# Kernel optimization log

Measured on AMD Instinct MI355X. Metric: run time of the kernel, lower is better.

The kernel has to match this reference:

```python
import jax, jax.numpy as jnp
import numpy as np

NQ, NL, NPCA, NCLS = 7, 6, 32, 3129
DIM = 2 ** NQ
B = 8192

# PauliZ diagonal per wire (PennyLane convention: wire 0 = most significant bit)
_bits = (np.arange(DIM)[None, :] >> (NQ - 1 - np.arange(NQ))[:, None]) & 1
Z_DIAG = jnp.asarray(1.0 - 2.0 * _bits, dtype=jnp.float32)  # (NQ, DIM)

# CNOT(control=q, target=(q+1)%NQ) as a static basis-index permutation (involution)
def _cnot_perm(c, t):
    idx = np.arange(DIM)
    cbit = (idx >> (NQ - 1 - c)) & 1
    return jnp.asarray(idx ^ (cbit << (NQ - 1 - t)))
CNOT_PERMS = [_cnot_perm(q, (q + 1) % NQ) for q in range(NQ)]

def _apply_ry(state, q, theta):
    # state: (B, DIM) complex64; theta: (B,) per-sample or scalar
    st = state.reshape(-1, 2 ** q, 2, 2 ** (NQ - 1 - q))
    th = jnp.asarray(theta)
    c = jnp.cos(th / 2)
    s = jnp.sin(th / 2)
    if th.ndim == 1:
        c = c[:, None, None]
        s = s[:, None, None]
    a0, a1 = st[:, :, 0, :], st[:, :, 1, :]
    return jnp.stack((c * a0 - s * a1, s * a0 + c * a1), axis=2).reshape(-1, DIM)

def _apply_rz(state, q, theta):
    # RZ = diag(e^{-i t/2}, e^{+i t/2}); theta is a shared scalar here
    st = state.reshape(-1, 2 ** q, 2, 2 ** (NQ - 1 - q))
    p = jnp.exp(jnp.complex64(-0.5j) * theta)
    a0, a1 = st[:, :, 0, :], st[:, :, 1, :]
    return jnp.stack((p * a0, jnp.conj(p) * a1), axis=2).reshape(-1, DIM)

def _quantum_circuit(feats, weights):
    # feats: (B, NL*NQ) encoding angles (data re-uploading); weights: (NL, NQ, 2)
    bsz = feats.shape[0]
    state = jnp.zeros((bsz, DIM), jnp.complex64).at[:, 0].set(1.0)
    for layer in range(NL):
        for q in range(NQ):
            # RY data-encoding followed by variational RY rotate about the same axis -> fuse angles
            state = _apply_ry(state, q, feats[:, layer * NQ + q] + weights[layer, q, 0])
            state = _apply_rz(state, q, weights[layer, q, 1])
        for q in range(NQ):  # ring entanglement
            state = state[:, CNOT_PERMS[q]]
    probs = state.real ** 2 + state.imag ** 2  # (B, DIM)
    return probs @ Z_DIAG.T  # (B, NQ) <Z_i> expectation values

def setup_inputs() -> dict:
    key = jax.random.key(0)
    ks = jax.random.split(key, 8)
    def lin(k, i, o):
        return (jax.random.normal(k, (i, o), jnp.float32) / np.sqrt(i)).astype(jnp.float32)
    return {
        "x": jax.random.normal(ks[0], (B, NPCA), jnp.float32),
        "feature_scale": jnp.ones((NPCA,), jnp.float32),
        "quantum_weights": jax.random.normal(ks[1], (NL, NQ, 2), jnp.float32) * 0.1,
        "qh_w1": lin(ks[2], NQ, 64), "qh_b1": jnp.zeros((64,), jnp.float32),
        "qh_w2": lin(ks[3], 64, NCLS), "qh_b2": jnp.zeros((NCLS,), jnp.float32),
        "ch_w1": lin(ks[4], NPCA, 256), "ch_b1": jnp.zeros((256,), jnp.float32),
        "ch_w2": lin(ks[5], 256, 128), "ch_b2": jnp.zeros((128,), jnp.float32),
        "ch_w3": lin(ks[6], 128, NCLS), "ch_b3": jnp.zeros((NCLS,), jnp.float32),
    }

def reference(x, feature_scale, quantum_weights, qh_w1, qh_b1, qh_w2, qh_b2,
              ch_w1, ch_b1, ch_w2, ch_b2, ch_w3, ch_b3):
    # prepare_features: learned scale -> arctan squash -> zero-pad to NL*NQ angles
    feats = jnp.arctan(x * feature_scale)
    feats = jnp.pad(feats, ((0, 0), (0, NL * NQ - NPCA)))
    q_features = _quantum_circuit(feats, quantum_weights)          # (B, NQ)
    q_logits = jax.nn.relu(q_features @ qh_w1 + qh_b1) @ qh_w2 + qh_b2
    h = jax.nn.relu(x @ ch_w1 + ch_b1)                             # dropout = identity at eval
    h = jax.nn.relu(h @ ch_w2 + ch_b2)
    c_logits = h @ ch_w3 + ch_b3
    return (q_logits, c_logits, q_features)
```

## Files before the change

kernel.cpp:

```cpp
#include <hip/hip_runtime.h>
#include <hip/hip_bf16.h>
#include <math.h>

#define NQ 7
#define NL 6
#define BATCH 8192
#define NPCA 32
#define NCLS 3129
#define NGATE 42

#define NBQ 2048
#define NBC 512
#define NBX 49
#define NBT (3 * NBX)

#define GXB 25
#define GYB 64
#define GNB (GXB * GYB * 2)
#define GCPX (GNB / 8)

typedef __attribute__((ext_vector_type(8))) short short8;
typedef __attribute__((ext_vector_type(4))) float f32x4;

__device__ __forceinline__ void gload_lds16(const void* g, void* l) {
    __builtin_amdgcn_global_load_lds(
        (const __attribute__((address_space(1))) void*)g,
        (__attribute__((address_space(3))) void*)l, 16, 0, 0);
}

__global__ __launch_bounds__(256) void prep_kernel(
    const float* __restrict__ x,
    const float* __restrict__ fscale,
    const float* __restrict__ qw,
    const float* __restrict__ qh_w1,
    const float* __restrict__ qh_b1,
    const float* __restrict__ cw1, const float* __restrict__ cb1,
    const float* __restrict__ cw2, const float* __restrict__ cb2,
    const float* __restrict__ qw2, const float* __restrict__ cw3,
    float* __restrict__ qf_out,
    __hip_bfloat16* __restrict__ hq_out,
    __hip_bfloat16* __restrict__ h2_out,
    __hip_bfloat16* __restrict__ qw2t,
    __hip_bfloat16* __restrict__ cw3t)
{
    __shared__ alignas(16) unsigned char smem[18752];
    const int bid = blockIdx.x;
    const int tid = threadIdx.x;

    if (bid < NBQ) {
        float* pzc = (float*)smem;
        float* pzs = pzc + NGATE;
        float* w0s = pzs + NGATE;
        if (tid < NGATE) {
            float t = qw[tid * 2 + 1] * 0.5f;
            float s, c;
            sincosf(t, &s, &c);
            pzs[tid] = s; pzc[tid] = c;
            w0s[tid] = qw[tid * 2 + 0];
        }
        __syncthreads();

        const int lane = tid & 63;
        const int wave = tid >> 6;
        const int sample = bid * 4 + wave;

        float myfeat = 0.f;
        if (lane < NPCA) myfeat = atanf(x[sample * NPCA + lane] * fscale[lane]);

        float rs[NGATE - NPCA], rc[NGATE - NPCA];
        #pragma unroll
        for (int g = NPCA; g < NGATE; ++g) {
            float th = w0s[g] * 0.5f;
            rs[g - NPCA] = __sinf(th);
            rc[g - NPCA] = __cosf(th);
        }

        float s0r = (lane == 0) ? 1.f : 0.f, s0i = 0.f, s1r = 0.f, s1i = 0.f;

        #pragma unroll
        for (int layer = 0; layer < NL; ++layer) {
            #pragma unroll
            for (int q = 0; q < NQ; ++q) {
                const int g = layer * NQ + q;
                const int b = NQ - 1 - q;
                float s, c;
                if (g < NPCA) {
                    float fv = __shfl(myfeat, g);
                    float th = (fv + w0s[g]) * 0.5f;
                    s = __sinf(th); c = __cosf(th);
                } else {
                    s = rs[g - NPCA]; c = rc[g - NPCA];
                }
                if (b == 0) {
                    float n0r = c * s0r - s * s1r, n0i = c * s0i - s * s1i;
                    float n1r = s * s0r + c * s1r, n1i = s * s0i + c * s1i;
                    s0r = n0r; s0i = n0i; s1r = n1r; s1i = n1i;
                } else {
                    int m = 1 << (b - 1);
                    float p0r = __shfl_xor(s0r, m), p0i = __shfl_xor(s0i, m);
                    float p1r = __shfl_xor(s1r, m), p1i = __shfl_xor(s1i, m);
                    if (((lane >> (b - 1)) & 1) == 0) {
                        s0r = c * s0r - s * p0r; s0i = c * s0i - s * p0i;
                        s1r = c * s1r - s * p1r; s1i = c * s1i - s * p1i;
                    } else {
                        s0r = s * p0r + c * s0r; s0i = s * p0i + c * s0i;
                        s1r = s * p1r + c * s1r; s1i = s * p1i + c * s1i;
                    }
                }
                float pc = pzc[g], ps = pzs[g];
                if (b == 0) {
                    float u0 = pc * s0r + ps * s0i; s0i = pc * s0i - ps * s0r; s0r = u0;
                    float u1 = pc * s1r - ps * s1i; s1i = pc * s1i + ps * s1r; s1r = u1;
                } else {
                    float e = (((lane >> (b - 1)) & 1) == 0) ? ps : -ps;
                    float u0 = pc * s0r + e * s0i; s0i = pc * s0i - e * s0r; s0r = u0;
                    float u1 = pc * s1r + e * s1i; s1i = pc * s1i - e * s1r; s1r = u1;
                }
            }
            #pragma unroll
            for (int cq = 0; cq < NQ; ++cq) {
                if (cq == NQ - 1) {
                    float r = __shfl_xor(s1r, 32), im = __shfl_xor(s1i, 32);
                    s1r = r; s1i = im;
                } else if (cq == NQ - 2) {
                    if (lane & 1) {
                        float tr = s0r; s0r = s1r; s1r = tr;
                        float ti = s0i; s0i = s1i; s1i = ti;
                    }
                } else {
                    const int bc = NQ - 1 - cq;
                    const int bt = bc - 1;
                    int m = 1 << (bt - 1);
                    float p0r = __shfl_xor(s0r, m), p0i = __shfl_xor(s0i, m);
                    float p1r = __shfl_xor(s1r, m), p1i = __shfl_xor(s1i, m);
                    if ((lane >> (bc - 1)) & 1) {
                        s0r = p0r; s0i = p0i; s1r = p1r; s1i = p1i;
                    }
                }
            }
        }

        float p0 = s0r * s0r + s0i * s0i;
        float p1 = s1r * s1r + s1i * s1i;
        float psum = p0 + p1;
        float qf[7];
        #pragma unroll
        for (int k = 0; k < 6; ++k)
            qf[k] = (((lane >> (5 - k)) & 1) ? -psum : psum);
        qf[6] = p0 - p1;
        #pragma unroll
        for (int off = 32; off >= 1; off >>= 1) {
            #pragma unroll
            for (int k = 0; k < 7; ++k) qf[k] += __shfl_xor(qf[k], off);
        }

        float acc = qh_b1[lane];
        #pragma unroll
        for (int k = 0; k < 7; ++k) acc += qf[k] * qh_w1[k * 64 + lane];
        hq_out[sample * 64 + lane] = __float2bfloat16(fmaxf(acc, 0.f));
        if (lane < 7) qf_out[sample * 7 + lane] = qf[lane];

    } else if (bid < NBQ + NBC) {
        float (*xs)[33]   = (float(*)[33])smem;
        float (*h1s)[260] = (float(*)[260])(smem + 2112);
        const int row0 = (bid - NBQ) * 16;

        for (int i = tid; i < 16 * 32; i += 256) {
            int r = i >> 5, k = i & 31;
            xs[r][k] = x[(row0 + r) * 32 + k];
        }
        __syncthreads();

        {
            float w1c[32];
            #pragma unroll
            for (int k = 0; k < 32; ++k) w1c[k] = cw1[k * 256 + tid];
            float bb = cb1[tid];
            #pragma unroll
            for (int r = 0; r < 16; ++r) {
                float a = bb;
                #pragma unroll
                for (int k = 0; k < 32; ++k) a += xs[r][k] * w1c[k];
                h1s[r][tid] = fmaxf(a, 0.f);
            }
        }
        __syncthreads();

        {
            const int c0 = (tid & 31) * 4;
            const int r0 = (tid >> 5) * 2;
            float4 bv = *(const float4*)&cb2[c0];
            float a0[4] = {bv.x, bv.y, bv.z, bv.w};
            float a1[4] = {bv.x, bv.y, bv.z, bv.w};
            for (int k = 0; k < 256; k += 4) {
                float4 h0 = *(const float4*)&h1s[r0][k];
                float4 h1 = *(const float4*)&h1s[r0 + 1][k];
                #pragma unroll
                for (int j = 0; j < 4; ++j) {
                    float4 w = *(const float4*)&cw2[(size_t)(k + j) * 128 + c0];
                    float hv0 = (j == 0) ? h0.x : (j == 1) ? h0.y : (j == 2) ? h0.z : h0.w;
                    float hv1 = (j == 0) ? h1.x : (j == 1) ? h1.y : (j == 2) ? h1.z : h1.w;
                    a0[0] += hv0 * w.x; a0[1] += hv0 * w.y; a0[2] += hv0 * w.z; a0[3] += hv0 * w.w;
                    a1[0] += hv1 * w.x; a1[1] += hv1 * w.y; a1[2] += hv1 * w.z; a1[3] += hv1 * w.w;
                }
            }
            #pragma unroll
            for (int rr = 0; rr < 2; ++rr) {
                float* a = rr ? a1 : a0;
                __hip_bfloat162 q0, q1;
                q0.x = __float2bfloat16(fmaxf(a[0], 0.f));
                q0.y = __float2bfloat16(fmaxf(a[1], 0.f));
                q1.x = __float2bfloat16(fmaxf(a[2], 0.f));
                q1.y = __float2bfloat16(fmaxf(a[3], 0.f));
                size_t base = (size_t)(row0 + r0 + rr) * 128 + c0;
                *(__hip_bfloat162*)&h2_out[base]     = q0;
                *(__hip_bfloat162*)&h2_out[base + 2] = q1;
            }
        }

    } else {
        float (*tile)[65] = (float(*)[65])smem;
        const int t = bid - (NBQ + NBC);
        const int y = t / NBX;
        const int n0 = (t % NBX) * 64;
        const float* W; __hip_bfloat16* Wt; int K, k0;
        if (y == 0) { W = qw2; Wt = qw2t; K = 64;  k0 = 0; }
        else        { W = cw3; Wt = cw3t; K = 128; k0 = (y - 1) * 64; }

        #pragma unroll
        for (int i = 0; i < 16; ++i) {
            int id = tid + i * 256;
            int kr = id >> 6, nc = id & 63;
            int n = n0 + nc;
            tile[kr][nc] = (n < NCLS) ? W[(size_t)(k0 + kr) * NCLS + n] : 0.f;
        }
        __syncthreads();
        #pragma unroll
        for (int i = 0; i < 16; ++i) {
            int id = tid + i * 256;
            int nr = id >> 6, kc = id & 63;
            int n = n0 + nr;
            if (n < NCLS) Wt[(size_t)n * K + k0 + kc] = __float2bfloat16(tile[kc][nr]);
        }
    }
}

__global__ __launch_bounds__(256) void gemm_mfma_dual(
    const __hip_bfloat16* __restrict__ A0, const __hip_bfloat16* __restrict__ B0,
    const float* __restrict__ bias0, float* __restrict__ C0,
    const __hip_bfloat16* __restrict__ A1, const __hip_bfloat16* __restrict__ B1,
    const float* __restrict__ bias1, float* __restrict__ C1, int N)
{
    __shared__ alignas(16) unsigned char shraw[32768];
    __hip_bfloat16* Alds = (__hip_bfloat16*)shraw;
    __hip_bfloat16* Blds = Alds + 128 * 64;
    float* scr = (float*)shraw;

    const int logical = (blockIdx.x & 7) * GCPX + (blockIdx.x >> 3);
    const int z   = logical >= (GXB * GYB);
    const int rem = logical - z * (GXB * GYB);
    const int by  = rem / GXB;
    const int bx  = rem - by * GXB;

    const __hip_bfloat16* A  = z ? A1 : A0;
    const __hip_bfloat16* Bt = z ? B1 : B0;
    const float* bias        = z ? bias1 : bias0;
    float* C                 = z ? C1 : C0;
    const int K              = z ? 128 : 64;

    const int tid  = threadIdx.x;
    const int lane = tid & 63;
    const int wave = tid >> 6;
    const int wr = wave >> 1, wc = wave & 1;
    const int row0 = by * 128;
    const int col0 = bx * 128;

    f32x4 acc[4][4] = {};

    for (int kb = 0; kb < K; kb += 64) {
        #pragma unroll
        for (int i = 0; i < 4; ++i) {
            int id = tid + i * 256;
            int r = id >> 3;
            int c = id & 7;
            int cs = c ^ (r & 7);
            gload_lds16(&A[(size_t)(row0 + r) * K + kb + cs * 8], &Alds[id * 8]);
        }
        #pragma unroll
        for (int i = 0; i < 4; ++i) {
            int id = tid + i * 256;
            int r = id >> 3;
            int c = id & 7;
            int cs = c ^ (r & 7);
            int n = col0 + r;
            if (n >= N) n = N - 1;
            gload_lds16(&Bt[(size_t)n * K + kb + cs * 8], &Blds[id * 8]);
        }
        __syncthreads();

        const int frow = lane & 15;
        const int chi  = lane >> 4;
        #pragma unroll
        for (int kk = 0; kk < 2; ++kk) {
            short8 af[4], bf[4];
            #pragma unroll
            for (int m = 0; m < 4; ++m) {
                int r = wr * 64 + m * 16 + frow;
                int cs = (kk * 4 + chi) ^ (r & 7);
                af[m] = *(const short8*)&Alds[r * 64 + cs * 8];
            }
            #pragma unroll
            for (int n = 0; n < 4; ++n) {
                int r = wc * 64 + n * 16 + frow;
                int cs = (kk * 4 + chi) ^ (r & 7);
                bf[n] = *(const short8*)&Blds[r * 64 + cs * 8];
            }
            #pragma unroll
            for (int m = 0; m < 4; ++m)
                #pragma unroll
                for (int n = 0; n < 4; ++n)
                    acc[m][n] = __builtin_amdgcn_mfma_f32_16x16x32_bf16(
                        af[m], bf[n], acc[m][n], 0, 0, 0);
        }
        __syncthreads();
    }

    const int g = lane >> 4;
    const int fcol = lane & 15;
    const int ccr = tid & 127;
    const int bc  = col0 + ccr;
    const float bv = (bc < N) ? bias[bc] : 0.f;

    #pragma unroll
    for (int p = 0; p < 2; ++p) {
        if (p) __syncthreads();
        #pragma unroll
        for (int mm = 0; mm < 2; ++mm) {
            #pragma unroll
            for (int n = 0; n < 4; ++n) {
                int rl = wr * 32 + mm * 16 + g * 4;
                int cc = wc * 64 + n * 16 + fcol;
                int ccs = cc ^ (((rl >> 2) & 1) << 4);
                #pragma unroll
                for (int r = 0; r < 4; ++r)
                    scr[(rl + r) * 128 + ccs] = acc[2 * p + mm][n][r];
            }
        }
        __syncthreads();
        if (bc < N) {
            #pragma unroll
            for (int i = 0; i < 32; ++i) {
                int id = i * 256 + tid;
                int rl = id >> 7;
                int ccs = ccr ^ (((rl >> 2) & 1) << 4);
                int grow = row0 + p * 32 + ((rl >> 5) << 6) + (rl & 31);
                C[(size_t)grow * N + bc] = scr[rl * 128 + ccs] + bv;
            }
        }
    }
}

extern "C" void kernel_launch(void* const* d_in, const int* in_sizes, int n_in,
                              void* d_out, int out_size, void* d_ws, size_t ws_size,
                              hipStream_t stream)
{
    const float* x   = (const float*)d_in[0];
    const float* fs  = (const float*)d_in[1];
    const float* qw  = (const float*)d_in[2];
    const float* qw1 = (const float*)d_in[3];
    const float* qb1 = (const float*)d_in[4];
    const float* qw2 = (const float*)d_in[5];
    const float* qb2 = (const float*)d_in[6];
    const float* cw1 = (const float*)d_in[7];
    const float* cb1 = (const float*)d_in[8];
    const float* cw2 = (const float*)d_in[9];
    const float* cb2 = (const float*)d_in[10];
    const float* cw3 = (const float*)d_in[11];
    const float* cb3 = (const float*)d_in[12];

    float* q_logits = (float*)d_out;
    float* c_logits = q_logits + (size_t)BATCH * NCLS;
    float* qf_out   = c_logits + (size_t)BATCH * NCLS;

    const int NPAD = 3200;
    __hip_bfloat16* hq   = (__hip_bfloat16*)d_ws;
    __hip_bfloat16* h2   = hq + (size_t)BATCH * 64;
    __hip_bfloat16* qw2t = h2 + (size_t)BATCH * 128;
    __hip_bfloat16* cw3t = qw2t + (size_t)NPAD * 64;

    prep_kernel<<<NBQ + NBC + NBT, 256, 0, stream>>>(
        x, fs, qw, qw1, qb1, cw1, cb1, cw2, cb2, qw2, cw3,
        qf_out, hq, h2, qw2t, cw3t);

    gemm_mfma_dual<<<GNB, 256, 0, stream>>>(hq, qw2t, qb2, q_logits,
                                            h2, cw3t, cb3, c_logits, NCLS);
}
```

Baseline: 96.49 us.

## Load MFMA operands directly from global memory instead of staging through LDS

The dual GEMM kernel no longer stages A and B tiles into shared memory with global_load_lds. Each wave now loads its bf16 MFMA fragments straight from global memory into registers. K is made a template parameter so the k-loop is fully unrolled for K=64 and K=128. This removes the LDS round trip and the barriers in the main loop. In exchange, operand rows are re-read by several waves through cache rather than shared once, and the loads are less coalesced (16-byte pieces spread across rows).

```diff
diff --git a/kernel.cpp b/kernel.cpp
--- a/kernel.cpp
+++ b/kernel.cpp
@@ -21,12 +21,6 @@
 
 typedef __attribute__((ext_vector_type(8))) short short8;
 typedef __attribute__((ext_vector_type(4))) float f32x4;
-
-__device__ __forceinline__ void gload_lds16(const void* g, void* l) {
-    __builtin_amdgcn_global_load_lds(
-        (const __attribute__((address_space(1))) void*)g,
-        (__attribute__((address_space(3))) void*)l, 16, 0, 0);
-}
 
 __global__ __launch_bounds__(256) void prep_kernel(
     const float* __restrict__ x,
@@ -245,84 +239,46 @@
     }
 }
 
-__global__ __launch_bounds__(256) void gemm_mfma_dual(
-    const __hip_bfloat16* __restrict__ A0, const __hip_bfloat16* __restrict__ B0,
-    const float* __restrict__ bias0, float* __restrict__ C0,
-    const __hip_bfloat16* __restrict__ A1, const __hip_bfloat16* __restrict__ B1,
-    const float* __restrict__ bias1, float* __restrict__ C1, int N)
+template <int K>
+__device__ __forceinline__ void gemm_body(
+    const __hip_bfloat16* __restrict__ A,
+    const __hip_bfloat16* __restrict__ Bt,
+    const float* __restrict__ bias,
+    float* __restrict__ C,
+    int N, int row0, int col0, int tid, float* scr)
 {
-    __shared__ alignas(16) unsigned char shraw[32768];
-    __hip_bfloat16* Alds = (__hip_bfloat16*)shraw;
-    __hip_bfloat16* Blds = Alds + 128 * 64;
-    float* scr = (float*)shraw;
-
-    const int logical = (blockIdx.x & 7) * GCPX + (blockIdx.x >> 3);
-    const int z   = logical >= (GXB * GYB);
-    const int rem = logical - z * (GXB * GYB);
-    const int by  = rem / GXB;
-    const int bx  = rem - by * GXB;
-
-    const __hip_bfloat16* A  = z ? A1 : A0;
-    const __hip_bfloat16* Bt = z ? B1 : B0;
-    const float* bias        = z ? bias1 : bias0;
-    float* C                 = z ? C1 : C0;
-    const int K              = z ? 128 : 64;
-
-    const int tid  = threadIdx.x;
     const int lane = tid & 63;
     const int wave = tid >> 6;
     const int wr = wave >> 1, wc = wave & 1;
-    const int row0 = by * 128;
-    const int col0 = bx * 128;
+    const int frow = lane & 15;
+    const int koff = (lane >> 4) << 3;
+
+    const __hip_bfloat16* aptr[4];
+    const __hip_bfloat16* bptr[4];
+    #pragma unroll
+    for (int m = 0; m < 4; ++m)
+        aptr[m] = &A[(size_t)(row0 + wr * 64 + m * 16 + frow) * K + koff];
+    #pragma unroll
+    for (int n = 0; n < 4; ++n) {
+        int nn = col0 + wc * 64 + n * 16 + frow;
+        if (nn >= N) nn = N - 1;
+        bptr[n] = &Bt[(size_t)nn * K + koff];
+    }
 
     f32x4 acc[4][4] = {};
-
-    for (int kb = 0; kb < K; kb += 64) {
-        #pragma unroll
-        for (int i = 0; i < 4; ++i) {
-            int id = tid + i * 256;
-            int r = id >> 3;
-            int c = id & 7;
-            int cs = c ^ (r & 7);
-            gload_lds16(&A[(size_t)(row0 + r) * K + kb + cs * 8], &Alds[id * 8]);
-        }
-        #pragma unroll
-        for (int i = 0; i < 4; ++i) {
-            int id = tid + i * 256;
-            int r = id >> 3;
-            int c = id & 7;
-            int cs = c ^ (r & 7);
-            int n = col0 + r;
-            if (n >= N) n = N - 1;
-            gload_lds16(&Bt[(size_t)n * K + kb + cs * 8], &Blds[id * 8]);
-        }
-        __syncthreads();
-
-        const int frow = lane & 15;
-        const int chi  = lane >> 4;
-        #pragma unroll
-        for (int kk = 0; kk < 2; ++kk) {
-            short8 af[4], bf[4];
-            #pragma unroll
-            for (int m = 0; m < 4; ++m) {
-                int r = wr * 64 + m * 16 + frow;
-                int cs = (kk * 4 + chi) ^ (r & 7);
-                af[m] = *(const short8*)&Alds[r * 64 + cs * 8];
-            }
-            #pragma unroll
-            for (int n = 0; n < 4; ++n) {
-                int r = wc * 64 + n * 16 + frow;
-                int cs = (kk * 4 + chi) ^ (r & 7);
-                bf[n] = *(const short8*)&Blds[r * 64 + cs * 8];
-            }
-            #pragma unroll
-            for (int m = 0; m < 4; ++m)
-                #pragma unroll
-                for (int n = 0; n < 4; ++n)
-                    acc[m][n] = __builtin_amdgcn_mfma_f32_16x16x32_bf16(
-                        af[m], bf[n], acc[m][n], 0, 0, 0);
-        }
-        __syncthreads();
+    #pragma unroll
+    for (int kk = 0; kk < K / 32; ++kk) {
+        short8 af[4], bf[4];
+        #pragma unroll
+        for (int m = 0; m < 4; ++m) af[m] = *(const short8*)(aptr[m] + kk * 32);
+        #pragma unroll
+        for (int n = 0; n < 4; ++n) bf[n] = *(const short8*)(bptr[n] + kk * 32);
+        #pragma unroll
+        for (int m = 0; m < 4; ++m)
+            #pragma unroll
+            for (int n = 0; n < 4; ++n)
+                acc[m][n] = __builtin_amdgcn_mfma_f32_16x16x32_bf16(
+                    af[m], bf[n], acc[m][n], 0, 0, 0);
     }
 
     const int g = lane >> 4;
@@ -358,6 +314,24 @@
             }
         }
     }
+}
+
+__global__ __launch_bounds__(256) void gemm_mfma_dual(
+    const __hip_bfloat16* __restrict__ A0, const __hip_bfloat16* __restrict__ B0,
+    const float* __restrict__ bias0, float* __restrict__ C0,
+    const __hip_bfloat16* __restrict__ A1, const __hip_bfloat16* __restrict__ B1,
+    const float* __restrict__ bias1, float* __restrict__ C1, int N)
+{
+    __shared__ float scr[64 * 128];
+
+    const int logical = (blockIdx.x & 7) * GCPX + (blockIdx.x >> 3);
+    const int z   = logical >= (GXB * GYB);
+    const int rem = logical - z * (GXB * GYB);
+    const int by  = rem / GXB;
+    const int bx  = rem - by * GXB;
+
+    if (z) gemm_body<128>(A1, B1, bias1, C1, N, by * 128, bx * 128, threadIdx.x, scr);
+    else   gemm_body<64> (A0, B0, bias0, C0, N, by * 128, bx * 128, threadIdx.x, scr);
 }
 
 extern "C" void kernel_launch(void* const* d_in, const int* in_sizes, int n_in,
```

Result: slower. 126.9 us (+31.5%).

## Store GEMM results directly from registers and interleave dual GEMMs per XCD

Applied to the files above, without the earlier changes.

The MFMA operands are swapped so each lane's accumulator holds four consecutive output columns. This lets the epilogue write float4 rows straight to global memory and drop the LDS scratch transpose along with its barriers. The K dimension becomes a template parameter, giving each of the two GEMMs its own specialised body. Block-to-tile mapping now interleaves the two problems within each XCD so both share cache locality. The output stores become less coalesced (16-byte chunks spread across rows) and rely on unaligned vector stores, since N=3129 is odd.

```diff
diff --git a/kernel.cpp b/kernel.cpp
--- a/kernel.cpp
+++ b/kernel.cpp
@@ -17,10 +17,11 @@
 #define GXB 25
 #define GYB 64
 #define GNB (GXB * GYB * 2)
-#define GCPX (GNB / 8)
+#define GPZX 200
 
 typedef __attribute__((ext_vector_type(8))) short short8;
 typedef __attribute__((ext_vector_type(4))) float f32x4;
+typedef __attribute__((ext_vector_type(4), aligned(4))) float f32x4u;
 
 __device__ __forceinline__ void gload_lds16(const void* g, void* l) {
     __builtin_amdgcn_global_load_lds(
@@ -245,35 +246,18 @@
     }
 }
 
-__global__ __launch_bounds__(256) void gemm_mfma_dual(
-    const __hip_bfloat16* __restrict__ A0, const __hip_bfloat16* __restrict__ B0,
-    const float* __restrict__ bias0, float* __restrict__ C0,
-    const __hip_bfloat16* __restrict__ A1, const __hip_bfloat16* __restrict__ B1,
-    const float* __restrict__ bias1, float* __restrict__ C1, int N)
+template <int K>
+__device__ __forceinline__ void gemm_body(
+    const __hip_bfloat16* __restrict__ A,
+    const __hip_bfloat16* __restrict__ Bt,
+    const float* __restrict__ bias,
+    float* __restrict__ C,
+    int N, int row0, int col0, int tid,
+    __hip_bfloat16* Alds, __hip_bfloat16* Blds)
 {
-    __shared__ alignas(16) unsigned char shraw[32768];
-    __hip_bfloat16* Alds = (__hip_bfloat16*)shraw;
-    __hip_bfloat16* Blds = Alds + 128 * 64;
-    float* scr = (float*)shraw;
-
-    const int logical = (blockIdx.x & 7) * GCPX + (blockIdx.x >> 3);
-    const int z   = logical >= (GXB * GYB);
-    const int rem = logical - z * (GXB * GYB);
-    const int by  = rem / GXB;
-    const int bx  = rem - by * GXB;
-
-    const __hip_bfloat16* A  = z ? A1 : A0;
-    const __hip_bfloat16* Bt = z ? B1 : B0;
-    const float* bias        = z ? bias1 : bias0;
-    float* C                 = z ? C1 : C0;
-    const int K              = z ? 128 : 64;
-
-    const int tid  = threadIdx.x;
     const int lane = tid & 63;
     const int wave = tid >> 6;
     const int wr = wave >> 1, wc = wave & 1;
-    const int row0 = by * 128;
-    const int col0 = bx * 128;
 
     f32x4 acc[4][4] = {};
 
@@ -316,48 +300,61 @@
                 bf[n] = *(const short8*)&Blds[r * 64 + cs * 8];
             }
             #pragma unroll
+            for (int n = 0; n < 4; ++n)
+                #pragma unroll
+                for (int m = 0; m < 4; ++m)
+                    acc[n][m] = __builtin_amdgcn_mfma_f32_16x16x32_bf16(
+                        bf[n], af[m], acc[n][m], 0, 0, 0);
+        }
+        __syncthreads();
+    }
+
+    const int mrow0 = row0 + wr * 64 + (lane & 15);
+    const int nc0   = col0 + wc * 64 + ((lane >> 4) << 2);
+    #pragma unroll
+    for (int n = 0; n < 4; ++n) {
+        int nc = nc0 + n * 16;
+        if (nc >= N) continue;
+        if (nc + 4 <= N) {
+            float4 bv = *(const float4*)&bias[nc];
+            #pragma unroll
+            for (int m = 0; m < 4; ++m) {
+                f32x4u v;
+                v[0] = acc[n][m][0] + bv.x;
+                v[1] = acc[n][m][1] + bv.y;
+                v[2] = acc[n][m][2] + bv.z;
+                v[3] = acc[n][m][3] + bv.w;
+                *(f32x4u*)&C[(size_t)(mrow0 + m * 16) * N + nc] = v;
+            }
+        } else {
+            #pragma unroll
             for (int m = 0; m < 4; ++m)
-                #pragma unroll
-                for (int n = 0; n < 4; ++n)
-                    acc[m][n] = __builtin_amdgcn_mfma_f32_16x16x32_bf16(
-                        af[m], bf[n], acc[m][n], 0, 0, 0);
-        }
-        __syncthreads();
+                for (int j = 0; j < 4; ++j)
+                    if (nc + j < N)
+                        C[(size_t)(mrow0 + m * 16) * N + nc + j] =
+                            acc[n][m][j] + bias[nc + j];
+        }
     }
-
-    const int g = lane >> 4;
-    const int fcol = lane & 15;
-    const int ccr = tid & 127;
-    const int bc  = col0 + ccr;
-    const float bv = (bc < N) ? bias[bc] : 0.f;
-
-    #pragma unroll
-    for (int p = 0; p < 2; ++p) {
-        if (p) __syncthreads();
-        #pragma unroll
-        for (int mm = 0; mm < 2; ++mm) {
-            #pragma unroll
-            for (int n = 0; n < 4; ++n) {
-                int rl = wr * 32 + mm * 16 + g * 4;
-                int cc = wc * 64 + n * 16 + fcol;
-                int ccs = cc ^ (((rl >> 2) & 1) << 4);
-                #pragma unroll
-                for (int r = 0; r < 4; ++r)
-                    scr[(rl + r) * 128 + ccs] = acc[2 * p + mm][n][r];
-            }
-        }
-        __syncthreads();
-        if (bc < N) {
-            #pragma unroll
-            for (int i = 0; i < 32; ++i) {
-                int id = i * 256 + tid;
-                int rl = id >> 7;
-                int ccs = ccr ^ (((rl >> 2) & 1) << 4);
-                int grow = row0 + p * 32 + ((rl >> 5) << 6) + (rl & 31);
-                C[(size_t)grow * N + bc] = scr[rl * 128 + ccs] + bv;
-            }
-        }
-    }
+}
+
+__global__ __launch_bounds__(256) void gemm_mfma_dual(
+    const __hip_bfloat16* __restrict__ A0, const __hip_bfloat16* __restrict__ B0,
+    const float* __restrict__ bias0, float* __restrict__ C0,
+    const __hip_bfloat16* __restrict__ A1, const __hip_bfloat16* __restrict__ B1,
+    const float* __restrict__ bias1, float* __restrict__ C1, int N)
+{
+    __shared__ __hip_bfloat16 Alds[128 * 64];
+    __shared__ __hip_bfloat16 Blds[128 * 64];
+
+    const int xcd = blockIdx.x & 7;
+    const int seq = blockIdx.x >> 3;
+    const int z   = seq & 1;
+    const int widx = xcd * GPZX + (seq >> 1);
+    const int by  = widx / GXB;
+    const int bx  = widx - by * GXB;
+
+    if (z) gemm_body<128>(A1, B1, bias1, C1, N, by * 128, bx * 128, threadIdx.x, Alds, Blds);
+    else   gemm_body<64> (A0, B0, bias0, C0, N, by * 128, bx * 128, threadIdx.x, Alds, Blds);
 }
 
 extern "C" void kernel_launch(void* const* d_in, const int* in_sizes, int n_in,
```

Result: slower. 126.9 us (+31.6%).
